# Optimization experiments

Hardware: AMD Instinct MI355X
Metric: run time of the kernel (lower is better)

Reference implementation:

```python
import jax, jax.numpy as jnp
import numpy as np

N = 50000       # nodes
E = 800000      # edges (avg degree 16)
C_IN = 128
C_OUT = 128
RATIO = 0.5
K = int(np.ceil(RATIO * N))  # static top-k size (single graph)
EPS = 1e-5      # BatchNorm eps


def setup_inputs() -> dict:
    key = jax.random.key(0)
    ks = jax.random.split(key, 12)
    x = jax.random.normal(ks[0], (N, C_IN), jnp.float32)
    edge_index = jax.random.randint(ks[1], (2, E), 0, N, dtype=jnp.int32)
    batch = jnp.zeros((N,), jnp.int32)
    s_in = 1.0 / np.sqrt(C_IN)
    s_out = 1.0 / np.sqrt(C_OUT)
    return {
        "x": x,
        "edge_index": edge_index,
        "batch": batch,
        "lin_w": jax.random.uniform(ks[2], (C_IN, C_OUT), jnp.float32, -s_in, s_in),
        "lin_b": jax.random.uniform(ks[3], (C_OUT,), jnp.float32, -s_in, s_in),
        "bn1_g": jnp.ones((C_OUT,), jnp.float32),
        "bn1_b": jnp.zeros((C_OUT,), jnp.float32),
        "gcn_w": jax.random.uniform(ks[4], (C_OUT, C_OUT), jnp.float32, -s_out, s_out),
        "gcn_b": jnp.zeros((C_OUT,), jnp.float32),
        "bn2_g": jnp.ones((C_OUT,), jnp.float32),
        "bn2_b": jnp.zeros((C_OUT,), jnp.float32),
        "pool_w": jax.random.uniform(ks[5], (C_OUT,), jnp.float32, -s_out, s_out),
    }


def _batchnorm(h, g, b):
    # training-mode BatchNorm1d: biased variance over the node axis
    mu = jnp.mean(h, axis=0)
    var = jnp.mean(jnp.square(h - mu), axis=0)
    return (h - mu) * jax.lax.rsqrt(var + EPS) * g + b


def reference(x, edge_index, batch, lin_w, lin_b, bn1_g, bn1_b,
              gcn_w, gcn_b, bn2_g, bn2_b, pool_w):
    # ---- MLP: Linear + BN + ReLU ----
    h = jax.nn.relu(_batchnorm(x @ lin_w + lin_b, bn1_g, bn1_b))

    # ---- GCNConv with self-loops + symmetric normalization ----
    loops = jnp.arange(N, dtype=edge_index.dtype)
    row = jnp.concatenate([edge_index[0], loops])  # source
    col = jnp.concatenate([edge_index[1], loops])  # target
    hw = h @ gcn_w                                    # [N, C_OUT]
    deg = jax.ops.segment_sum(jnp.ones_like(col, jnp.float32), col, num_segments=N)
    dinv = jnp.where(deg > 0, jax.lax.rsqrt(deg), 0.0)
    norm = dinv[row] * dinv[col]                      # [E+N]
    agg = jax.ops.segment_sum(hw[row] * norm[:, None], col, num_segments=N)
    out = agg + gcn_b

    # ---- BN + ReLU ----
    h2 = jax.nn.relu(_batchnorm(out, bn2_g, bn2_b))

    # ---- TopKPooling (single graph -> static k) ----
    score = jnp.tanh((h2 @ pool_w) / jnp.linalg.norm(pool_w))
    top_score, perm = jax.lax.top_k(score, K)
    x_pool = h2[perm] * top_score[:, None]            # [K, C_OUT]
    batch_new = batch[perm]

    # filter_adj with fixed shape: dropped edges marked -1
    mask = jnp.zeros((N,), bool).at[perm].set(True)
    new_idx = jnp.full((N,), -1, edge_index.dtype).at[perm].set(
        jnp.arange(K, dtype=edge_index.dtype))
    src, dst = edge_index[0], edge_index[1]
    keep = mask[src] & mask[dst]
    ei_new = jnp.where(keep[None, :],
                       jnp.stack([new_idx[src], new_idx[dst]]),
                       jnp.array(-1, edge_index.dtype))
    return x_pool, ei_new, batch_new
```

## Files before the change

### kernel.cpp

```cpp
#include <hip/hip_runtime.h>
#include <hip/hip_bf16.h>

#define NN 50000
#define EE 800000
#define KTOP 25000
#define EPSF 1e-5

__global__ __launch_bounds__(256, 2) void gemm_bn_stats(const float* __restrict__ A,
                                                        const float* __restrict__ W,
                                                        const float* __restrict__ bias,
                                                        float* __restrict__ Y,
                                                        double* __restrict__ part, int M) {
    __shared__ float Bs[128][128];
    __shared__ float As[32][132];
    int t = threadIdx.x;
    int bm = blockIdx.x * 128;

    const float4* W4 = (const float4*)W;
    float4* Bs4 = (float4*)Bs;
#pragma unroll
    for (int i = 0; i < 16; i++) Bs4[t + i * 256] = W4[t + i * 256];

    float acc[8][8];
#pragma unroll
    for (int i = 0; i < 8; i++)
#pragma unroll
        for (int j = 0; j < 8; j++) acc[i][j] = 0.f;

    int ty = t >> 4;
    int tx = t & 15;

    for (int kc = 0; kc < 4; kc++) {
        __syncthreads();
#pragma unroll
        for (int i = 0; i < 4; i++) {
            int f4 = t + i * 256;
            int r = f4 >> 3, k4 = f4 & 7;
            int row = bm + r;
            float4 v = make_float4(0.f, 0.f, 0.f, 0.f);
            if (row < M) v = *(const float4*)&A[(size_t)row * 128 + kc * 32 + k4 * 4];
            As[k4 * 4 + 0][r] = v.x;
            As[k4 * 4 + 1][r] = v.y;
            As[k4 * 4 + 2][r] = v.z;
            As[k4 * 4 + 3][r] = v.w;
        }
        __syncthreads();
#pragma unroll
        for (int kk = 0; kk < 32; kk++) {
            float4 a0 = *(float4*)&As[kk][ty * 8];
            float4 a1 = *(float4*)&As[kk][ty * 8 + 4];
            float4 b0 = *(float4*)&Bs[kc * 32 + kk][tx * 4];
            float4 b1 = *(float4*)&Bs[kc * 32 + kk][64 + tx * 4];
            float av[8] = {a0.x, a0.y, a0.z, a0.w, a1.x, a1.y, a1.z, a1.w};
            float bv[8] = {b0.x, b0.y, b0.z, b0.w, b1.x, b1.y, b1.z, b1.w};
#pragma unroll
            for (int i = 0; i < 8; i++)
#pragma unroll
                for (int j = 0; j < 8; j++) acc[i][j] += av[i] * bv[j];
        }
    }

    float4 bb0 = *(const float4*)&bias[tx * 4];
    float4 bb1 = *(const float4*)&bias[64 + tx * 4];
    float s[8], s2[8];
#pragma unroll
    for (int j = 0; j < 8; j++) { s[j] = 0.f; s2[j] = 0.f; }
#pragma unroll
    for (int i = 0; i < 8; i++) {
        int row = bm + ty * 8 + i;
        if (row < M) {
            float4 y0, y1;
            y0.x = acc[i][0] + bb0.x; y0.y = acc[i][1] + bb0.y;
            y0.z = acc[i][2] + bb0.z; y0.w = acc[i][3] + bb0.w;
            y1.x = acc[i][4] + bb1.x; y1.y = acc[i][5] + bb1.y;
            y1.z = acc[i][6] + bb1.z; y1.w = acc[i][7] + bb1.w;
            *(float4*)&Y[(size_t)row * 128 + tx * 4] = y0;
            *(float4*)&Y[(size_t)row * 128 + 64 + tx * 4] = y1;
            s[0] += y0.x; s2[0] += y0.x * y0.x;
            s[1] += y0.y; s2[1] += y0.y * y0.y;
            s[2] += y0.z; s2[2] += y0.z * y0.z;
            s[3] += y0.w; s2[3] += y0.w * y0.w;
            s[4] += y1.x; s2[4] += y1.x * y1.x;
            s[5] += y1.y; s2[5] += y1.y * y1.y;
            s[6] += y1.z; s2[6] += y1.z * y1.z;
            s[7] += y1.w; s2[7] += y1.w * y1.w;
        }
    }
    __syncthreads();
    float2* Sred = (float2*)As;
#pragma unroll
    for (int j = 0; j < 8; j++) {
        int col = (j < 4) ? (tx * 4 + j) : (64 + tx * 4 + j - 4);
        Sred[ty * 128 + col] = make_float2(s[j], s2[j]);
    }
    __syncthreads();
    if (t < 128) {
        double S = 0.0, S2 = 0.0;
#pragma unroll
        for (int r = 0; r < 16; r++) {
            float2 v = Sred[r * 128 + t];
            S += (double)v.x;
            S2 += (double)v.y;
        }
        part[((size_t)blockIdx.x * 128 + t) * 2 + 0] = S;
        part[((size_t)blockIdx.x * 128 + t) * 2 + 1] = S2;
    }
}

__global__ __launch_bounds__(256, 2) void gemm_bn_apply(const float* __restrict__ Yin,
                                                        const float* __restrict__ W,
                                                        const float* __restrict__ sc,
                                                        const float* __restrict__ sh,
                                                        const float* __restrict__ dinv,
                                                        float* __restrict__ HWs, int M) {
    __shared__ float Bs[128][128];
    __shared__ float As[32][132];
    int t = threadIdx.x;
    int bm = blockIdx.x * 128;

    const float4* W4 = (const float4*)W;
    float4* Bs4 = (float4*)Bs;
#pragma unroll
    for (int i = 0; i < 16; i++) Bs4[t + i * 256] = W4[t + i * 256];

    float acc[8][8];
#pragma unroll
    for (int i = 0; i < 8; i++)
#pragma unroll
        for (int j = 0; j < 8; j++) acc[i][j] = 0.f;

    int ty = t >> 4;
    int tx = t & 15;

    for (int kc = 0; kc < 4; kc++) {
        __syncthreads();
#pragma unroll
        for (int i = 0; i < 4; i++) {
            int f4 = t + i * 256;
            int r = f4 >> 3, k4 = f4 & 7;
            int row = bm + r;
            int col = kc * 32 + k4 * 4;
            float4 v = make_float4(0.f, 0.f, 0.f, 0.f);
            if (row < M) {
                float4 y = *(const float4*)&Yin[(size_t)row * 128 + col];
                float4 scv = *(const float4*)&sc[col];
                float4 shv = *(const float4*)&sh[col];
                v.x = fmaxf(y.x * scv.x + shv.x, 0.f);
                v.y = fmaxf(y.y * scv.y + shv.y, 0.f);
                v.z = fmaxf(y.z * scv.z + shv.z, 0.f);
                v.w = fmaxf(y.w * scv.w + shv.w, 0.f);
            }
            As[k4 * 4 + 0][r] = v.x;
            As[k4 * 4 + 1][r] = v.y;
            As[k4 * 4 + 2][r] = v.z;
            As[k4 * 4 + 3][r] = v.w;
        }
        __syncthreads();
#pragma unroll
        for (int kk = 0; kk < 32; kk++) {
            float4 a0 = *(float4*)&As[kk][ty * 8];
            float4 a1 = *(float4*)&As[kk][ty * 8 + 4];
            float4 b0 = *(float4*)&Bs[kc * 32 + kk][tx * 4];
            float4 b1 = *(float4*)&Bs[kc * 32 + kk][64 + tx * 4];
            float av[8] = {a0.x, a0.y, a0.z, a0.w, a1.x, a1.y, a1.z, a1.w};
            float bv[8] = {b0.x, b0.y, b0.z, b0.w, b1.x, b1.y, b1.z, b1.w};
#pragma unroll
            for (int i = 0; i < 8; i++)
#pragma unroll
                for (int j = 0; j < 8; j++) acc[i][j] += av[i] * bv[j];
        }
    }
#pragma unroll
    for (int i = 0; i < 8; i++) {
        int row = bm + ty * 8 + i;
        if (row < M) {
            float di = dinv[row];
            float4 o0, o1;
            o0.x = acc[i][0] * di; o0.y = acc[i][1] * di;
            o0.z = acc[i][2] * di; o0.w = acc[i][3] * di;
            o1.x = acc[i][4] * di; o1.y = acc[i][5] * di;
            o1.z = acc[i][6] * di; o1.w = acc[i][7] * di;
            *(float4*)&HWs[(size_t)row * 128 + tx * 4] = o0;
            *(float4*)&HWs[(size_t)row * 128 + 64 + tx * 4] = o1;
        }
    }
}

__global__ __launch_bounds__(256) void bn_finalize(const double* __restrict__ part, int nb,
                                                   const float* __restrict__ g,
                                                   const float* __restrict__ beta,
                                                   float* __restrict__ scale,
                                                   float* __restrict__ shift, int M) {
    int c = blockIdx.x;
    int t = threadIdx.x;
    double s = 0.0, s2 = 0.0;
    for (int b = t; b < nb; b += 256) {
        s += part[((size_t)b * 128 + c) * 2 + 0];
        s2 += part[((size_t)b * 128 + c) * 2 + 1];
    }
    __shared__ double sd[256], sd2[256];
    sd[t] = s;
    sd2[t] = s2;
    __syncthreads();
#pragma unroll
    for (int o = 128; o > 0; o >>= 1) {
        if (t < o) {
            sd[t] += sd[t + o];
            sd2[t] += sd2[t + o];
        }
        __syncthreads();
    }
    if (t == 0) {
        double S = sd[0], S2 = sd2[0];
        double mu = S / (double)M;
        double var = S2 / (double)M - mu * mu;
        double inv = 1.0 / sqrt(var + (double)EPSF);
        scale[c] = (float)((double)g[c] * inv);
        shift[c] = (float)((double)beta[c] - mu * (double)g[c] * inv);
    }
}

__global__ __launch_bounds__(256) void bn_finalize2(const float2* __restrict__ part, int nb,
                                                    const float* __restrict__ g,
                                                    const float* __restrict__ beta,
                                                    float* __restrict__ scale,
                                                    float* __restrict__ shift, int M) {
    int c = blockIdx.x;
    int t = threadIdx.x;
    double s = 0.0, s2 = 0.0;
    for (int b = t; b < nb; b += 256) {
        float2 v = part[(size_t)b * 128 + c];
        s += (double)v.x;
        s2 += (double)v.y;
    }
    __shared__ double sd[256], sd2[256];
    sd[t] = s;
    sd2[t] = s2;
    __syncthreads();
#pragma unroll
    for (int o = 128; o > 0; o >>= 1) {
        if (t < o) {
            sd[t] += sd[t + o];
            sd2[t] += sd2[t + o];
        }
        __syncthreads();
    }
    if (t == 0) {
        double S = sd[0], S2 = sd2[0];
        double mu = S / (double)M;
        double var = S2 / (double)M - mu * mu;
        double inv = 1.0 / sqrt(var + (double)EPSF);
        scale[c] = (float)((double)g[c] * inv);
        shift[c] = (float)((double)beta[c] - mu * (double)g[c] * inv);
    }
}

__global__ __launch_bounds__(256) void count_deg(const int* __restrict__ col,
                                                 int* __restrict__ cnt, int E) {
    int e = blockIdx.x * 256 + threadIdx.x;
    if (e < E) atomicAdd(&cnt[col[e]], 1);
}

__global__ __launch_bounds__(256) void fill_csr(const int* __restrict__ row,
                                                const int* __restrict__ col,
                                                const int* __restrict__ off,
                                                int* __restrict__ cur,
                                                int* __restrict__ csr, int E) {
    int e = blockIdx.x * 256 + threadIdx.x;
    if (e < E) {
        int c = col[e];
        int p = atomicAdd(&cur[c], 1);
        csr[off[c] + p] = row[e];
    }
}

__device__ __forceinline__ int waveInclScan(int v, int lane) {
#pragma unroll
    for (int o = 1; o < 64; o <<= 1) {
        int u = __shfl_up(v, o, 64);
        if (lane >= o) v += u;
    }
    return v;
}

__global__ __launch_bounds__(1024) void scan_phase1(const int* __restrict__ in,
                                                    int* __restrict__ out,
                                                    int* __restrict__ bsum,
                                                    float* __restrict__ dinv, int n) {
    int t = threadIdx.x;
    int g = blockIdx.x * 1024 + t;
    int lane = t & 63, wid = t >> 6;
    int v = (g < n) ? in[g] : 0;
    if (dinv && g < n) dinv[g] = (float)(1.0 / sqrt((double)(v + 1)));
    int incl = waveInclScan(v, lane);
    __shared__ int ws[16];
    if (lane == 63) ws[wid] = incl;
    __syncthreads();
    if (t < 16) {
        int x = ws[t];
#pragma unroll
        for (int o = 1; o < 16; o <<= 1) {
            int u = __shfl_up(x, o, 64);
            if (t >= o) x += u;
        }
        ws[t] = x;
    }
    __syncthreads();
    int pre = (wid > 0) ? ws[wid - 1] : 0;
    if (g < n) out[g] = pre + incl - v;
    if (t == 1023) bsum[blockIdx.x] = ws[15];
}

__global__ __launch_bounds__(1024) void scan_phase2(int* __restrict__ bsum, int B,
                                                    int* __restrict__ out, int n) {
    int t = threadIdx.x;
    int lane = t & 63, wid = t >> 6;
    int v = (t < B) ? bsum[t] : 0;
    int incl = waveInclScan(v, lane);
    __shared__ int ws[16];
    if (lane == 63) ws[wid] = incl;
    __syncthreads();
    if (t < 16) {
        int x = ws[t];
#pragma unroll
        for (int o = 1; o < 16; o <<= 1) {
            int u = __shfl_up(x, o, 64);
            if (t >= o) x += u;
        }
        ws[t] = x;
    }
    __syncthreads();
    int pre = (wid > 0) ? ws[wid - 1] : 0;
    int glob_incl = pre + incl;
    if (t < B) bsum[t] = glob_incl - v;
    if (t == B - 1) out[n] = glob_incl;
}

__global__ __launch_bounds__(1024) void scan_phase3(int* __restrict__ out,
                                                    const int* __restrict__ bsum, int n) {
    int g = blockIdx.x * 1024 + threadIdx.x;
    if (g < n) out[g] += bsum[blockIdx.x];
}

__global__ __launch_bounds__(512) void gcn_agg(const float* __restrict__ HWs,
                                               const int* __restrict__ off,
                                               const int* __restrict__ csr,
                                               const float* __restrict__ dinv,
                                               const float* __restrict__ gcn_b,
                                               float* __restrict__ OUT,
                                               float2* __restrict__ part32, int M) {
    int t = threadIdx.x;
    int w = t >> 6;
    int lane = t & 63;
    int half = lane >> 5;
    int l32 = lane & 31;
    int i = blockIdx.x * 8 + w;

    const float4* H4 = (const float4*)HWs;
    double a0 = 0.0, a1 = 0.0, a2 = 0.0, a3 = 0.0;

    if (i < M) {
        int o0 = off[i], o1 = off[i + 1];
        if (half == 0) {
            float4 sv = H4[(size_t)i * 32 + l32];
            a0 = sv.x; a1 = sv.y; a2 = sv.z; a3 = sv.w;
        }
        int e = o0;
        for (; e + 4 <= o1; e += 4) {
            int sA = csr[e + half];
            int sB = csr[e + 2 + half];
            float4 vA = H4[(size_t)sA * 32 + l32];
            float4 vB = H4[(size_t)sB * 32 + l32];
            a0 += (double)vA.x + (double)vB.x;
            a1 += (double)vA.y + (double)vB.y;
            a2 += (double)vA.z + (double)vB.z;
            a3 += (double)vA.w + (double)vB.w;
        }
        if (e + 2 <= o1) {
            int sA = csr[e + half];
            float4 vA = H4[(size_t)sA * 32 + l32];
            a0 += (double)vA.x; a1 += (double)vA.y;
            a2 += (double)vA.z; a3 += (double)vA.w;
            e += 2;
        }
        if (e < o1 && half == 0) {
            int sA = csr[e];
            float4 vA = H4[(size_t)sA * 32 + l32];
            a0 += (double)vA.x; a1 += (double)vA.y;
            a2 += (double)vA.z; a3 += (double)vA.w;
        }
    }
    a0 += __shfl_down(a0, 32, 64);
    a1 += __shfl_down(a1, 32, 64);
    a2 += __shfl_down(a2, 32, 64);
    a3 += __shfl_down(a3, 32, 64);

    __shared__ float2 sred[8][128];
    if (i < M && half == 0) {
        double di = (double)dinv[i];
        float4 gb = ((const float4*)gcn_b)[l32];
        float4 y;
        y.x = (float)(a0 * di) + gb.x;
        y.y = (float)(a1 * di) + gb.y;
        y.z = (float)(a2 * di) + gb.z;
        y.w = (float)(a3 * di) + gb.w;
        ((float4*)OUT)[(size_t)i * 32 + l32] = y;
        sred[w][l32 * 4 + 0] = make_float2(y.x, y.x * y.x);
        sred[w][l32 * 4 + 1] = make_float2(y.y, y.y * y.y);
        sred[w][l32 * 4 + 2] = make_float2(y.z, y.z * y.z);
        sred[w][l32 * 4 + 3] = make_float2(y.w, y.w * y.w);
    }
    __syncthreads();
    if (t < 128) {
        float S = 0.f, S2 = 0.f;
#pragma unroll
        for (int ww = 0; ww < 8; ww++) {
            float2 v = sred[ww][t];
            S += v.x;
            S2 += v.y;
        }
        part32[(size_t)blockIdx.x * 128 + t] = make_float2(S, S2);
    }
}

__global__ __launch_bounds__(256) void score_key(const float* __restrict__ Y2,
                                                 const float* __restrict__ sc,
                                                 const float* __restrict__ sh,
                                                 const float* __restrict__ w,
                                                 float* __restrict__ score,
                                                 unsigned* __restrict__ key,
                                                 int* __restrict__ bcnt, int M) {
    int lane = threadIdx.x & 63;
    int wid = threadIdx.x >> 6;
    int gw = blockIdx.x * 4 + wid;
    int nw = gridDim.x * 4;

    float w0 = w[lane], w1 = w[lane + 64];
    float sc0 = sc[lane], sh0 = sh[lane];
    float sc1 = sc[lane + 64], sh1 = sh[lane + 64];

    float nv = w0 * w0 + w1 * w1;
#pragma unroll
    for (int o = 32; o >= 1; o >>= 1) nv += __shfl_xor(nv, o, 64);
    float nrm = sqrtf(nv);

    for (int r = gw; r < M; r += nw) {
        float a = Y2[(size_t)r * 128 + lane];
        float b = Y2[(size_t)r * 128 + lane + 64];
        a = fmaxf(a * sc0 + sh0, 0.f);
        b = fmaxf(b * sc1 + sh1, 0.f);
        float v = a * w0 + b * w1;
#pragma unroll
        for (int o = 32; o >= 1; o >>= 1) v += __shfl_xor(v, o, 64);
        if (lane == 0) {
            score[r] = tanhf(v / nrm);
            unsigned u = __float_as_uint(v);
            unsigned k = (u & 0x80000000u) ? ~u : (u | 0x80000000u);
            key[r] = k;
            atomicAdd(&bcnt[k >> 16], 1);
        }
    }
}

__global__ __launch_bounds__(256) void bucket_fill(const unsigned* __restrict__ key,
                                                   const int* __restrict__ boff,
                                                   int* __restrict__ bcur,
                                                   int* __restrict__ bmem, int M) {
    int i = blockIdx.x * 256 + threadIdx.x;
    if (i < M) {
        int b = key[i] >> 16;
        int p = atomicAdd(&bcur[b], 1);
        bmem[boff[b] + p] = i;
    }
}

__global__ __launch_bounds__(256) void rank_kernel(const unsigned* __restrict__ key,
                                                   const int* __restrict__ boff,
                                                   const int* __restrict__ bmem,
                                                   int* __restrict__ rank,
                                                   int* __restrict__ nidx, int M) {
    int i = blockIdx.x * 256 + threadIdx.x;
    if (i >= M) return;
    unsigned ki = key[i];
    int b = ki >> 16;
    int r = M - boff[b + 1];
    int p0 = boff[b], p1 = boff[b + 1];
    for (int p = p0; p < p1; p++) {
        int j = bmem[p];
        unsigned kj = key[j];
        if (kj > ki || (kj == ki && j < i)) r++;
    }
    rank[i] = r;
    nidx[i] = (r < KTOP) ? r : -1;
}

__global__ __launch_bounds__(128) void write_pool(const float* __restrict__ Y2,
                                                  const float* __restrict__ sc,
                                                  const float* __restrict__ sh,
                                                  const float* __restrict__ score,
                                                  const int* __restrict__ rank,
                                                  float* __restrict__ out0,
                                                  float* __restrict__ out2, int M) {
    int sub = threadIdx.x >> 5;
    int c4 = threadIdx.x & 31;
    int i = blockIdx.x * 4 + sub;
    if (i >= M) return;
    int r = rank[i];
    if (r < KTOP) {
        float s = score[i];
        float4 y = *(const float4*)&Y2[(size_t)i * 128 + c4 * 4];
        float4 scv = *(const float4*)&sc[c4 * 4];
        float4 shv = *(const float4*)&sh[c4 * 4];
        float4 o;
        o.x = fmaxf(y.x * scv.x + shv.x, 0.f) * s;
        o.y = fmaxf(y.y * scv.y + shv.y, 0.f) * s;
        o.z = fmaxf(y.z * scv.z + shv.z, 0.f) * s;
        o.w = fmaxf(y.w * scv.w + shv.w, 0.f) * s;
        *(float4*)&out0[(size_t)r * 128 + c4 * 4] = o;
        if (c4 == 0) out2[r] = 0.0f;
    }
}

__global__ __launch_bounds__(256) void write_edges(const int* __restrict__ row,
                                                   const int* __restrict__ col,
                                                   const int* __restrict__ nidx,
                                                   float* __restrict__ out1, int E) {
    int e = blockIdx.x * 256 + threadIdx.x;
    if (e < E) {
        int a = nidx[row[e]];
        int b = nidx[col[e]];
        bool keep = (a >= 0) && (b >= 0);
        out1[e] = keep ? (float)a : -1.0f;
        out1[E + e] = keep ? (float)b : -1.0f;
    }
}

extern "C" void kernel_launch(void* const* d_in, const int* in_sizes, int n_in,
                              void* d_out, int out_size, void* d_ws, size_t ws_size,
                              hipStream_t stream) {
    const float* x = (const float*)d_in[0];
    const int* ei = (const int*)d_in[1];
    const float* lin_w = (const float*)d_in[3];
    const float* lin_b = (const float*)d_in[4];
    const float* bn1_g = (const float*)d_in[5];
    const float* bn1_b = (const float*)d_in[6];
    const float* gcn_w = (const float*)d_in[7];
    const float* gcn_b = (const float*)d_in[8];
    const float* bn2_g = (const float*)d_in[9];
    const float* bn2_b = (const float*)d_in[10];
    const float* pool_w = (const float*)d_in[11];

    const int* e_row = ei;
    const int* e_col = ei + EE;

    char* ws = (char*)d_ws;
    size_t off_b = 0;
    auto alloc = [&](size_t bytes) -> void* {
        void* p = ws + off_b;
        off_b = (off_b + bytes + 255) & ~(size_t)255;
        return p;
    };
    float* y = (float*)alloc((size_t)NN * 128 * 4);
    float* hws = (float*)alloc((size_t)NN * 128 * 4);
    int* cnt = (int*)alloc(NN * 4);
    int* cur = (int*)alloc(NN * 4);
    int* offs = (int*)alloc((NN + 1) * 4);
    float* dinv = (float*)alloc(NN * 4);
    int* csr = (int*)alloc((size_t)EE * 4);
    float* score = (float*)alloc(NN * 4);
    unsigned* key = (unsigned*)alloc(NN * 4);
    int* rank = (int*)alloc(NN * 4);
    int* nidx = (int*)alloc(NN * 4);
    int* bcnt = (int*)alloc(65536 * 4);
    int* bcur = (int*)alloc(65536 * 4);
    int* boff = (int*)alloc((65536 + 1) * 4);
    int* bmem = (int*)alloc(NN * 4);
    double* part = (double*)alloc((size_t)400 * 128 * 2 * 8);
    float* scale1 = (float*)alloc(128 * 4);
    float* shift1 = (float*)alloc(128 * 4);
    float* scale2 = (float*)alloc(128 * 4);
    float* shift2 = (float*)alloc(128 * 4);
    int* bsum = (int*)alloc(128 * 4);

    float* out0 = (float*)d_out;
    float* out1 = out0 + (size_t)KTOP * 128;
    float* out2 = out1 + (size_t)2 * EE;

    float2* part32 = (float2*)out0;
    int gcn_grid = (NN + 7) / 8;

    int gemm_grid = (NN + 127) / 128;

    hipMemsetAsync(cnt, 0, (size_t)((char*)cur - (char*)cnt) + NN * 4, stream);
    hipMemsetAsync(bcnt, 0, (size_t)((char*)bcur - (char*)bcnt) + 65536 * 4, stream);
    count_deg<<<(EE + 255) / 256, 256, 0, stream>>>(e_col, cnt, EE);
    {
        int B = (NN + 1023) / 1024;
        scan_phase1<<<B, 1024, 0, stream>>>(cnt, offs, bsum, dinv, NN);
        scan_phase2<<<1, 1024, 0, stream>>>(bsum, B, offs, NN);
        scan_phase3<<<B, 1024, 0, stream>>>(offs, bsum, NN);
    }
    fill_csr<<<(EE + 255) / 256, 256, 0, stream>>>(e_row, e_col, offs, cur, csr, EE);

    gemm_bn_stats<<<gemm_grid, 256, 0, stream>>>(x, lin_w, lin_b, y, part, NN);
    bn_finalize<<<128, 256, 0, stream>>>(part, gemm_grid, bn1_g, bn1_b, scale1, shift1, NN);

    gemm_bn_apply<<<gemm_grid, 256, 0, stream>>>(y, gcn_w, scale1, shift1, dinv, hws, NN);
    gcn_agg<<<gcn_grid, 512, 0, stream>>>(hws, offs, csr, dinv, gcn_b, y, part32, NN);

    bn_finalize2<<<128, 256, 0, stream>>>(part32, gcn_grid, bn2_g, bn2_b, scale2, shift2, NN);

    score_key<<<512, 256, 0, stream>>>(y, scale2, shift2, pool_w, score, key, bcnt, NN);
    {
        int B = 65536 / 1024;
        scan_phase1<<<B, 1024, 0, stream>>>(bcnt, boff, bsum, nullptr, 65536);
        scan_phase2<<<1, 1024, 0, stream>>>(bsum, B, boff, 65536);
        scan_phase3<<<B, 1024, 0, stream>>>(boff, bsum, 65536);
    }
    bucket_fill<<<(NN + 255) / 256, 256, 0, stream>>>(key, boff, bcur, bmem, NN);
    rank_kernel<<<(NN + 255) / 256, 256, 0, stream>>>(key, boff, bmem, rank, nidx, NN);

    write_pool<<<(NN + 3) / 4, 128, 0, stream>>>(y, scale2, shift2, score, rank, out0, out2, NN);
    write_edges<<<(EE + 255) / 256, 256, 0, stream>>>(e_row, e_col, nidx, out1, EE);
}
```

Baseline: 366.4 us.

## Merge small kernels, widen top-k buckets, pack keys in bucket storage

Several launch-reducing changes: the bucket-count memset is folded into count_deg, scan phases 2 and 3 are merged into a single one-block kernel, and write_pool/write_edges are combined into one launch. The top-k radix bucketing moves from 16 to 18 bits (shift 14) so buckets hold fewer keys, and bucket storage keeps (key,index) pairs so rank_kernel avoids an indirect key lookup. The gcn_agg stats reduction is reorganised into float4 shared arrays. The trade-off is that the single-block phase-3 pass over 262144 entries is serial, and the larger bucket arrays must now be zeroed and scanned.

Result: no change. 370.9 us (+1.2%).

```diff
diff --git a/kernel.cpp b/kernel.cpp
--- a/kernel.cpp
+++ b/kernel.cpp
@@ -5,6 +5,8 @@
 #define EE 800000
 #define KTOP 25000
 #define EPSF 1e-5
+#define NB (1 << 18)
+#define KSHIFT 14
 
 __global__ __launch_bounds__(256, 2) void gemm_bn_stats(const float* __restrict__ A,
                                                         const float* __restrict__ W,
@@ -256,8 +258,10 @@
 }
 
 __global__ __launch_bounds__(256) void count_deg(const int* __restrict__ col,
-                                                 int* __restrict__ cnt, int E) {
+                                                 int* __restrict__ cnt,
+                                                 int* __restrict__ zbase, int zn, int E) {
     int e = blockIdx.x * 256 + threadIdx.x;
+    if (e < zn) zbase[e] = 0;
     if (e < E) atomicAdd(&cnt[col[e]], 1);
 }
 
@@ -311,8 +315,8 @@
     if (t == 1023) bsum[blockIdx.x] = ws[15];
 }
 
-__global__ __launch_bounds__(1024) void scan_phase2(int* __restrict__ bsum, int B,
-                                                    int* __restrict__ out, int n) {
+__global__ __launch_bounds__(1024) void scan_phase23(const int* __restrict__ bsum, int B,
+                                                     int* __restrict__ out, int n) {
     int t = threadIdx.x;
     int lane = t & 63, wid = t >> 6;
     int v = (t < B) ? bsum[t] : 0;
@@ -331,15 +335,11 @@
     }
     __syncthreads();
     int pre = (wid > 0) ? ws[wid - 1] : 0;
-    int glob_incl = pre + incl;
-    if (t < B) bsum[t] = glob_incl - v;
-    if (t == B - 1) out[n] = glob_incl;
-}
-
-__global__ __launch_bounds__(1024) void scan_phase3(int* __restrict__ out,
-                                                    const int* __restrict__ bsum, int n) {
-    int g = blockIdx.x * 1024 + threadIdx.x;
-    if (g < n) out[g] += bsum[blockIdx.x];
+    __shared__ int sb[1024];
+    if (t < B) sb[t] = pre + incl - v;
+    if (t == B - 1) out[n] = pre + incl;
+    __syncthreads();
+    for (int idx = t; idx < n; idx += 1024) out[idx] += sb[idx >> 10];
 }
 
 __global__ __launch_bounds__(512) void gcn_agg(const float* __restrict__ HWs,
@@ -395,29 +395,34 @@
     a2 += __shfl_down(a2, 32, 64);
     a3 += __shfl_down(a3, 32, 64);
 
-    __shared__ float2 sred[8][128];
-    if (i < M && half == 0) {
-        double di = (double)dinv[i];
-        float4 gb = ((const float4*)gcn_b)[l32];
-        float4 y;
-        y.x = (float)(a0 * di) + gb.x;
-        y.y = (float)(a1 * di) + gb.y;
-        y.z = (float)(a2 * di) + gb.z;
-        y.w = (float)(a3 * di) + gb.w;
-        ((float4*)OUT)[(size_t)i * 32 + l32] = y;
-        sred[w][l32 * 4 + 0] = make_float2(y.x, y.x * y.x);
-        sred[w][l32 * 4 + 1] = make_float2(y.y, y.y * y.y);
-        sred[w][l32 * 4 + 2] = make_float2(y.z, y.z * y.z);
-        sred[w][l32 * 4 + 3] = make_float2(y.w, y.w * y.w);
+    __shared__ float4 sredS[8][32];
+    __shared__ float4 sredQ[8][32];
+    if (half == 0) {
+        if (i < M) {
+            double di = (double)dinv[i];
+            float4 gb = ((const float4*)gcn_b)[l32];
+            float4 y;
+            y.x = (float)(a0 * di) + gb.x;
+            y.y = (float)(a1 * di) + gb.y;
+            y.z = (float)(a2 * di) + gb.z;
+            y.w = (float)(a3 * di) + gb.w;
+            ((float4*)OUT)[(size_t)i * 32 + l32] = y;
+            sredS[w][l32] = y;
+            sredQ[w][l32] = make_float4(y.x * y.x, y.y * y.y, y.z * y.z, y.w * y.w);
+        } else {
+            sredS[w][l32] = make_float4(0.f, 0.f, 0.f, 0.f);
+            sredQ[w][l32] = make_float4(0.f, 0.f, 0.f, 0.f);
+        }
     }
     __syncthreads();
     if (t < 128) {
+        const float* fS = (const float*)sredS;
+        const float* fQ = (const float*)sredQ;
         float S = 0.f, S2 = 0.f;
 #pragma unroll
         for (int ww = 0; ww < 8; ww++) {
-            float2 v = sred[ww][t];
-            S += v.x;
-            S2 += v.y;
+            S += fS[ww * 128 + t];
+            S2 += fQ[ww * 128 + t];
         }
         part32[(size_t)blockIdx.x * 128 + t] = make_float2(S, S2);
     }
@@ -457,7 +462,7 @@
             unsigned u = __float_as_uint(v);
             unsigned k = (u & 0x80000000u) ? ~u : (u | 0x80000000u);
             key[r] = k;
-            atomicAdd(&bcnt[k >> 16], 1);
+            atomicAdd(&bcnt[k >> KSHIFT], 1);
         }
     }
 }
@@ -465,73 +470,78 @@
 __global__ __launch_bounds__(256) void bucket_fill(const unsigned* __restrict__ key,
                                                    const int* __restrict__ boff,
                                                    int* __restrict__ bcur,
-                                                   int* __restrict__ bmem, int M) {
+                                                   uint2* __restrict__ bmem, int M) {
     int i = blockIdx.x * 256 + threadIdx.x;
     if (i < M) {
-        int b = key[i] >> 16;
+        unsigned k = key[i];
+        int b = k >> KSHIFT;
         int p = atomicAdd(&bcur[b], 1);
-        bmem[boff[b] + p] = i;
+        bmem[boff[b] + p] = make_uint2(k, (unsigned)i);
     }
 }
 
 __global__ __launch_bounds__(256) void rank_kernel(const unsigned* __restrict__ key,
                                                    const int* __restrict__ boff,
-                                                   const int* __restrict__ bmem,
+                                                   const uint2* __restrict__ bmem,
                                                    int* __restrict__ rank,
                                                    int* __restrict__ nidx, int M) {
     int i = blockIdx.x * 256 + threadIdx.x;
     if (i >= M) return;
     unsigned ki = key[i];
-    int b = ki >> 16;
+    int b = ki >> KSHIFT;
     int r = M - boff[b + 1];
     int p0 = boff[b], p1 = boff[b + 1];
     for (int p = p0; p < p1; p++) {
-        int j = bmem[p];
-        unsigned kj = key[j];
-        if (kj > ki || (kj == ki && j < i)) r++;
+        uint2 kj = bmem[p];
+        if (kj.x > ki || (kj.x == ki && (int)kj.y < i)) r++;
     }
     rank[i] = r;
     nidx[i] = (r < KTOP) ? r : -1;
 }
 
-__global__ __launch_bounds__(128) void write_pool(const float* __restrict__ Y2,
-                                                  const float* __restrict__ sc,
-                                                  const float* __restrict__ sh,
-                                                  const float* __restrict__ score,
-                                                  const int* __restrict__ rank,
-                                                  float* __restrict__ out0,
-                                                  float* __restrict__ out2, int M) {
-    int sub = threadIdx.x >> 5;
-    int c4 = threadIdx.x & 31;
-    int i = blockIdx.x * 4 + sub;
-    if (i >= M) return;
-    int r = rank[i];
-    if (r < KTOP) {
-        float s = score[i];
-        float4 y = *(const float4*)&Y2[(size_t)i * 128 + c4 * 4];
-        float4 scv = *(const float4*)&sc[c4 * 4];
-        float4 shv = *(const float4*)&sh[c4 * 4];
-        float4 o;
-        o.x = fmaxf(y.x * scv.x + shv.x, 0.f) * s;
-        o.y = fmaxf(y.y * scv.y + shv.y, 0.f) * s;
-        o.z = fmaxf(y.z * scv.z + shv.z, 0.f) * s;
-        o.w = fmaxf(y.w * scv.w + shv.w, 0.f) * s;
-        *(float4*)&out0[(size_t)r * 128 + c4 * 4] = o;
-        if (c4 == 0) out2[r] = 0.0f;
-    }
-}
-
-__global__ __launch_bounds__(256) void write_edges(const int* __restrict__ row,
-                                                   const int* __restrict__ col,
-                                                   const int* __restrict__ nidx,
-                                                   float* __restrict__ out1, int E) {
-    int e = blockIdx.x * 256 + threadIdx.x;
-    if (e < E) {
-        int a = nidx[row[e]];
-        int b = nidx[col[e]];
-        bool keep = (a >= 0) && (b >= 0);
-        out1[e] = keep ? (float)a : -1.0f;
-        out1[E + e] = keep ? (float)b : -1.0f;
+#define MPB ((NN + 7) / 8)
+#define EB ((EE + 255) / 256)
+
+__global__ __launch_bounds__(256) void write_all(const float* __restrict__ Y2,
+                                                 const float* __restrict__ sc,
+                                                 const float* __restrict__ sh,
+                                                 const float* __restrict__ score,
+                                                 const int* __restrict__ rank,
+                                                 const int* __restrict__ erow,
+                                                 const int* __restrict__ ecol,
+                                                 const int* __restrict__ nidx,
+                                                 float* __restrict__ out0,
+                                                 float* __restrict__ out1,
+                                                 float* __restrict__ out2, int M, int E) {
+    int blk = blockIdx.x;
+    if (blk < MPB) {
+        int sub = threadIdx.x >> 5;
+        int c4 = threadIdx.x & 31;
+        int i = blk * 8 + sub;
+        if (i >= M) return;
+        int r = rank[i];
+        if (r < KTOP) {
+            float s = score[i];
+            float4 y = *(const float4*)&Y2[(size_t)i * 128 + c4 * 4];
+            float4 scv = *(const float4*)&sc[c4 * 4];
+            float4 shv = *(const float4*)&sh[c4 * 4];
+            float4 o;
+            o.x = fmaxf(y.x * scv.x + shv.x, 0.f) * s;
+            o.y = fmaxf(y.y * scv.y + shv.y, 0.f) * s;
+            o.z = fmaxf(y.z * scv.z + shv.z, 0.f) * s;
+            o.w = fmaxf(y.w * scv.w + shv.w, 0.f) * s;
+            *(float4*)&out0[(size_t)r * 128 + c4 * 4] = o;
+            if (c4 == 0) out2[r] = 0.0f;
+        }
+    } else {
+        int e = (blk - MPB) * 256 + threadIdx.x;
+        if (e < E) {
+            int a = nidx[erow[e]];
+            int b = nidx[ecol[e]];
+            bool keep = (a >= 0) && (b >= 0);
+            out1[e] = keep ? (float)a : -1.0f;
+            out1[E + e] = keep ? (float)b : -1.0f;
+        }
     }
 }
 
@@ -571,16 +581,16 @@
     unsigned* key = (unsigned*)alloc(NN * 4);
     int* rank = (int*)alloc(NN * 4);
     int* nidx = (int*)alloc(NN * 4);
-    int* bcnt = (int*)alloc(65536 * 4);
-    int* bcur = (int*)alloc(65536 * 4);
-    int* boff = (int*)alloc((65536 + 1) * 4);
-    int* bmem = (int*)alloc(NN * 4);
+    int* bcnt = (int*)alloc((size_t)NB * 4);
+    int* bcur = (int*)alloc((size_t)NB * 4);
+    int* boff = (int*)alloc(((size_t)NB + 1) * 4);
+    uint2* bmem = (uint2*)alloc((size_t)NN * 8);
     double* part = (double*)alloc((size_t)400 * 128 * 2 * 8);
     float* scale1 = (float*)alloc(128 * 4);
     float* shift1 = (float*)alloc(128 * 4);
     float* scale2 = (float*)alloc(128 * 4);
     float* shift2 = (float*)alloc(128 * 4);
-    int* bsum = (int*)alloc(128 * 4);
+    int* bsum = (int*)alloc(256 * 4);
 
     float* out0 = (float*)d_out;
     float* out1 = out0 + (size_t)KTOP * 128;
@@ -588,17 +598,14 @@
 
     float2* part32 = (float2*)out0;
     int gcn_grid = (NN + 7) / 8;
-
     int gemm_grid = (NN + 127) / 128;
 
     hipMemsetAsync(cnt, 0, (size_t)((char*)cur - (char*)cnt) + NN * 4, stream);
-    hipMemsetAsync(bcnt, 0, (size_t)((char*)bcur - (char*)bcnt) + 65536 * 4, stream);
-    count_deg<<<(EE + 255) / 256, 256, 0, stream>>>(e_col, cnt, EE);
+    count_deg<<<(EE + 255) / 256, 256, 0, stream>>>(e_col, cnt, bcnt, 2 * NB, EE);
     {
         int B = (NN + 1023) / 1024;
         scan_phase1<<<B, 1024, 0, stream>>>(cnt, offs, bsum, dinv, NN);
-        scan_phase2<<<1, 1024, 0, stream>>>(bsum, B, offs, NN);
-        scan_phase3<<<B, 1024, 0, stream>>>(offs, bsum, NN);
+        scan_phase23<<<1, 1024, 0, stream>>>(bsum, B, offs, NN);
     }
     fill_csr<<<(EE + 255) / 256, 256, 0, stream>>>(e_row, e_col, offs, cur, csr, EE);
 
@@ -612,14 +619,13 @@
 
     score_key<<<512, 256, 0, stream>>>(y, scale2, shift2, pool_w, score, key, bcnt, NN);
     {
-        int B = 65536 / 1024;
-        scan_phase1<<<B, 1024, 0, stream>>>(bcnt, boff, bsum, nullptr, 65536);
-        scan_phase2<<<1, 1024, 0, stream>>>(bsum, B, boff, 65536);
-        scan_phase3<<<B, 1024, 0, stream>>>(boff, bsum, 65536);
+        int B = NB / 1024;
+        scan_phase1<<<B, 1024, 0, stream>>>(bcnt, boff, bsum, nullptr, NB);
+        scan_phase23<<<1, 1024, 0, stream>>>(bsum, B, boff, NB);
     }
     bucket_fill<<<(NN + 255) / 256, 256, 0, stream>>>(key, boff, bcur, bmem, NN);
     rank_kernel<<<(NN + 255) / 256, 256, 0, stream>>>(key, boff, bmem, rank, nidx, NN);
 
-    write_pool<<<(NN + 3) / 4, 128, 0, stream>>>(y, scale2, shift2, score, rank, out0, out2, NN);
-    write_edges<<<(EE + 255) / 256, 256, 0, stream>>>(e_row, e_col, nidx, out1, EE);
-}
+    write_all<<<MPB + EB, 256, 0, stream>>>(y, scale2, shift2, score, rank,
+                                            e_row, e_col, nidx, out0, out1, out2, NN, EE);
+}
```
